# Optimization experiments

Measured on AMD Instinct MI355X. Metric: run time of the kernel, lower is better.

## Reference

```python
import jax, jax.numpy as jnp
import numpy as np
from jax import lax

STRIDES = (8, 16, 32)
NUM_CLASSES = 80
REG_MAX = 16
CONF_THR = 0.25
IOU_THR = 0.7
MAX_DET = 300
MAX_WH = 7680.0  # class-id offset for class-aware NMS


def setup_inputs() -> dict:
    key = jax.random.key(0)
    k1, k2, k3 = jax.random.split(key, 3)
    B = 32
    C = 4 * REG_MAX + NUM_CLASSES  # 144
    return {
        "p3": jax.random.normal(k1, (B, 80, 80, C), jnp.float32),
        "p4": jax.random.normal(k2, (B, 40, 40, C), jnp.float32),
        "p5": jax.random.normal(k3, (B, 20, 20, C), jnp.float32),
    }


def _make_anchors(shapes, strides):
    pts, strs = [], []
    for (h, w), s in zip(shapes, strides):
        sx = jnp.arange(w, dtype=jnp.float32) + 0.5
        sy = jnp.arange(h, dtype=jnp.float32) + 0.5
        gy, gx = jnp.meshgrid(sy, sx, indexing="ij")
        pts.append(jnp.stack([gx.ravel(), gy.ravel()], 0))  # (2, h*w)
        strs.append(jnp.full((h * w,), float(s), jnp.float32))
    return jnp.concatenate(pts, 1), jnp.concatenate(strs, 0)  # (2,A), (A,)


def _pairwise_iou(a, b):
    # a: (K,4) xyxy, b: (K,4) xyxy -> (K,K)
    lt = jnp.maximum(a[:, None, :2], b[None, :, :2])
    rb = jnp.minimum(a[:, None, 2:], b[None, :, 2:])
    wh = jnp.clip(rb - lt, 0.0)
    inter = wh[..., 0] * wh[..., 1]
    aa = (a[:, 2] - a[:, 0]) * (a[:, 3] - a[:, 1])
    ab = (b[:, 2] - b[:, 0]) * (b[:, 3] - b[:, 1])
    return inter / (aa[:, None] + ab[None, :] - inter + 1e-7)


def _nms_single(pred):
    # pred: (A, 4+nc) with boxes in xywh (center) format, scores sigmoid-activated
    xywh = pred[:, :4]
    scores = pred[:, 4:]
    best = jnp.max(scores, axis=-1)
    cls = jnp.argmax(scores, axis=-1)
    half = xywh[:, 2:] * 0.5
    boxes = jnp.concatenate([xywh[:, :2] - half, xywh[:, :2] + half], -1)  # xyxy
    score = jnp.where(best > CONF_THR, best, 0.0)
    top_s, idx = lax.top_k(score, MAX_DET)
    cbox = boxes[idx]                      # (K,4)
    ccls = cls[idx]                        # (K,)
    obox = cbox + ccls.astype(cbox.dtype)[:, None] * MAX_WH  # class-aware offset
    iou = _pairwise_iou(obox, obox)        # (K,K)
    k = jnp.arange(MAX_DET)

    def body(keep, i):
        suppressed = jnp.any(keep & (iou[i] > IOU_THR) & (k < i))
        ki = (top_s[i] > 0.0) & (~suppressed)
        return keep.at[i].set(ki), None

    keep, _ = lax.scan(body, jnp.zeros((MAX_DET,), bool), k)
    det = jnp.concatenate([cbox, top_s[:, None], ccls[:, None].astype(jnp.float32)], -1)
    return jnp.where(keep[:, None], det, 0.0)  # (K, 6): x1,y1,x2,y2,conf,cls


def _forward(p3, p4, p5):
    feats = [p3, p4, p5]
    shapes = [(f.shape[1], f.shape[2]) for f in feats]
    B = p3.shape[0]
    C = 4 * REG_MAX + NUM_CLASSES
    x = jnp.concatenate([f.reshape(B, -1, C) for f in feats], axis=1)  # (B, A, 144)
    box = x[:, :, : 4 * REG_MAX]   # (B, A, 64)
    cls = x[:, :, 4 * REG_MAX:]    # (B, A, 80)
    # DFL: split 64 channels into 4 sides x 16 bins, softmax over bins, expectation
    probs = jax.nn.softmax(box.reshape(B, -1, 4, REG_MAX), axis=-1)
    bins = jnp.arange(REG_MAX, dtype=jnp.float32)
    dist = jnp.einsum("bakr,r->bak", probs, bins)  # (B, A, 4) = l,t,r,b distances
    anchors, stride = _make_anchors(shapes, STRIDES)
    anc = anchors.T[None]  # (1, A, 2) anchor centers in grid units
    x1y1 = anc - dist[:, :, :2]
    x2y2 = anc + dist[:, :, 2:]
    dbox = jnp.concatenate([(x1y1 + x2y2) * 0.5, x2y2 - x1y1], -1) * stride[None, :, None]
    return jnp.concatenate([dbox, jax.nn.sigmoid(cls)], -1)  # (B, A, 84)


def reference(p3, p4, p5):
    pred = _forward(p3, p4, p5)
    return jax.vmap(_nms_single)(pred)  # (B, MAX_DET, 6)
```

## Files before the change

### kernel.cpp

```cpp
#include <hip/hip_runtime.h>
#include <math.h>

#define NUM_CLASSES 80
#define REG_MAX 16
#define NCH 144
#define A_TOT 8400
#define BATCH 32
#define MAX_DET 300
#define CONF_THR 0.25f
#define IOU_THR 0.7f
#define MAX_WH 7680.0f
#define CAP 1024
#define NBINS 1024
#define MASK_W 10
#define MROW 324

__global__ __launch_bounds__(256) void score_kernel(
    const float* __restrict__ p3, const float* __restrict__ p4,
    const float* __restrict__ p5,
    float* __restrict__ scores, int* __restrict__ clsArr)
{
    const int t = blockIdx.x * 256 + threadIdx.x;
    const int g = t >> 2;
    const int p = t & 3;
    const int b = g / A_TOT;
    const int a = g - b * A_TOT;

    const float* src;
    if (a < 6400)      src = p3 + ((size_t)b * 6400 + a) * NCH;
    else if (a < 8000) src = p4 + ((size_t)b * 1600 + (a - 6400)) * NCH;
    else               src = p5 + ((size_t)b * 400  + (a - 8000)) * NCH;

    const float4* s4 = (const float4*)src;
    float best = -INFINITY;
    int cbest = p * 4;
    #pragma unroll
    for (int q = 0; q < 5; ++q) {
        float4 c4 = s4[16 + q * 4 + p];
        int c = q * 16 + p * 4;
        if (c4.x > best) { best = c4.x; cbest = c + 0; }
        if (c4.y > best) { best = c4.y; cbest = c + 1; }
        if (c4.z > best) { best = c4.z; cbest = c + 2; }
        if (c4.w > best) { best = c4.w; cbest = c + 3; }
    }
    #pragma unroll
    for (int d = 1; d < 4; d <<= 1) {
        float ob = __shfl_xor(best, d, 64);
        int   oc = __shfl_xor(cbest, d, 64);
        if (ob > best || (ob == best && oc < cbest)) { best = ob; cbest = oc; }
    }

    if (p == 0) {
        float sig = 1.0f / (1.0f + expf(-best));
        scores[g] = (sig > CONF_THR) ? sig : 0.0f;
        clsArr[g] = cbest;
    }
}

__global__ __launch_bounds__(1024, 4) void nms_fused_kernel(
    const float* __restrict__ p3, const float* __restrict__ p4,
    const float* __restrict__ p5,
    const float* __restrict__ scores, const int* __restrict__ clsArr,
    float* __restrict__ out)
{
    __shared__ float sc_l[A_TOT];
    __shared__ unsigned hist[NBINS];
    __shared__ unsigned wtot[16];
    __shared__ unsigned woff[16];
    __shared__ unsigned long long cand[CAP];
    __shared__ unsigned long long sortedK[MAX_DET];
    __shared__ float4 cbox4[MAX_DET];
    __shared__ float4 obox4[MAX_DET];
    __shared__ float oarea[MAX_DET];
    __shared__ float tops[MAX_DET];
    __shared__ float tcls[MAX_DET];
    __shared__ unsigned mask[MASK_W][MROW];
    __shared__ unsigned aliveW[MASK_W];
    __shared__ unsigned keepW[MASK_W];
    __shared__ int bstar;
    __shared__ unsigned cnt;

    const int b = blockIdx.x;
    const int tid = threadIdx.x;
    const int lane = tid & 63;
    const int wv = tid >> 6;
    const float* sc = scores + (size_t)b * A_TOT;
    const int* cl = clsArr + (size_t)b * A_TOT;

    hist[tid] = 0;
    if (tid < MAX_DET) sortedK[tid] = 0ULL;
    if (tid == 0) { cnt = 0u; bstar = 0; }
    __syncthreads();

    #pragma unroll
    for (int k = 0; k < 9; ++k) {
        int i = tid + k * 1024;
        if (i < A_TOT) {
            float s = sc[i];
            sc_l[i] = s;
            if (s > 0.0f) {
                int bin = min((int)(s * (float)NBINS), NBINS - 1);
                atomicAdd(&hist[bin], 1u);
            }
        }
    }
    __syncthreads();

    unsigned v = hist[tid];
    #pragma unroll
    for (int d = 1; d < 64; d <<= 1) {
        unsigned o = __shfl_down(v, d, 64);
        if (lane + d < 64) v += o;
    }
    if (lane == 0) wtot[wv] = v;
    __syncthreads();
    if (tid < 16) {
        unsigned u = wtot[tid];
        unsigned t2 = u;
        #pragma unroll
        for (int d = 1; d < 16; d <<= 1) {
            unsigned o = __shfl_down(t2, d, 64);
            if (tid + d < 16) t2 += o;
        }
        woff[tid] = t2 - u;
    }
    __syncthreads();
    unsigned suff = v + woff[wv];
    hist[tid] = suff;
    __syncthreads();

    if (hist[tid] >= MAX_DET && (tid == NBINS - 1 || hist[tid + 1] < MAX_DET))
        bstar = tid;
    __syncthreads();
    const int bs = bstar;

    #pragma unroll
    for (int k = 0; k < 9; ++k) {
        int i = tid + k * 1024;
        float s = (i < A_TOT) ? sc_l[i] : 0.0f;
        bool pass = false;
        if (s > 0.0f) {
            int bin = min((int)(s * (float)NBINS), NBINS - 1);
            pass = (bin >= bs);
        }
        unsigned long long mb = __ballot(pass);
        unsigned nw = (unsigned)__popcll(mb);
        unsigned base = 0u;
        if (lane == 0) base = nw ? atomicAdd(&cnt, nw) : 0u;
        base = __shfl(base, 0, 64);
        if (pass) {
            unsigned off = (unsigned)__popcll(mb & ((1ULL << lane) - 1ULL));
            unsigned pos = base + off;
            if (pos < CAP) {
                unsigned sb = __float_as_uint(s);
                cand[pos] = ((unsigned long long)sb << 32) |
                            (unsigned long long)(0xFFFFFFFFu - (unsigned)i);
            }
        }
    }
    __syncthreads();

    const int n = min((int)cnt, CAP);
    if (tid < n) {
        unsigned long long mykey = cand[tid];
        int r = 0;
        #pragma unroll 8
        for (int j = 0; j < n; ++j) r += (cand[j] > mykey) ? 1 : 0;
        if (r < MAX_DET) sortedK[r] = mykey;
    }
    __syncthreads();

    const int gbase = lane & ~3;
    #pragma unroll
    for (int sweep = 0; sweep < 2; ++sweep) {
        int det = sweep * 256 + (tid >> 2);
        int p = tid & 3;
        unsigned long long key = (det < MAX_DET) ? sortedK[det] : 0ULL;
        float distp = 0.0f;
        unsigned i = 0xFFFFFFFFu - (unsigned)(key & 0xFFFFFFFFull);

        if (key != 0ULL) {
            const float* rowp;
            if (i < 6400)      rowp = p3 + ((size_t)b * 6400 + i) * NCH;
            else if (i < 8000) rowp = p4 + ((size_t)b * 1600 + (i - 6400)) * NCH;
            else               rowp = p5 + ((size_t)b * 400  + (i - 8000)) * NCH;
            const float4* s4 = (const float4*)rowp;
            float vv[16];
            float4 r0 = s4[p * 4 + 0];
            float4 r1 = s4[p * 4 + 1];
            float4 r2 = s4[p * 4 + 2];
            float4 r3 = s4[p * 4 + 3];
            vv[0]=r0.x; vv[1]=r0.y; vv[2]=r0.z; vv[3]=r0.w;
            vv[4]=r1.x; vv[5]=r1.y; vv[6]=r1.z; vv[7]=r1.w;
            vv[8]=r2.x; vv[9]=r2.y; vv[10]=r2.z; vv[11]=r2.w;
            vv[12]=r3.x; vv[13]=r3.y; vv[14]=r3.z; vv[15]=r3.w;
            float m = vv[0];
            #pragma unroll
            for (int k = 1; k < 16; ++k) m = fmaxf(m, vv[k]);
            float ssum = 0.0f, wsum = 0.0f;
            #pragma unroll
            for (int k = 0; k < 16; ++k) {
                float e = expf(vv[k] - m);
                ssum += e;
                wsum += e * (float)k;
            }
            distp = wsum / ssum;
        }
        float d0 = __shfl(distp, gbase + 0, 64);
        float d1 = __shfl(distp, gbase + 1, 64);
        float d2 = __shfl(distp, gbase + 2, 64);
        float d3 = __shfl(distp, gbase + 3, 64);

        if (det < MAX_DET && p == 0) {
            float s = __uint_as_float((unsigned)(key >> 32));
            tops[det] = s;
            float4 bb = make_float4(0.f, 0.f, 0.f, 0.f);
            float4 ob = bb;
            float cf = 0.0f;
            if (key != 0ULL) {
                int gyi, gxi; float strd;
                if (i < 6400)      { gyi = i / 80; gxi = i - gyi * 80; strd = 8.0f; }
                else if (i < 8000) { int li = i - 6400; gyi = li / 40; gxi = li - gyi * 40; strd = 16.0f; }
                else               { int li = i - 8000; gyi = li / 20; gxi = li - gyi * 20; strd = 32.0f; }
                float gx = (float)gxi + 0.5f;
                float gy = (float)gyi + 0.5f;
                float x1 = gx - d0, y1 = gy - d1;
                float x2 = gx + d2, y2 = gy + d3;
                float cx = ((x1 + x2) * 0.5f) * strd;
                float cy = ((y1 + y2) * 0.5f) * strd;
                float bw = (x2 - x1) * strd;
                float bh = (y2 - y1) * strd;
                float hx = bw * 0.5f, hy = bh * 0.5f;
                bb = make_float4(cx - hx, cy - hy, cx + hx, cy + hy);
                cf = (float)cl[i];
                float off = cf * MAX_WH;
                ob = make_float4(bb.x + off, bb.y + off, bb.z + off, bb.w + off);
            }
            cbox4[det] = bb;
            obox4[det] = ob;
            tcls[det] = cf;
            oarea[det] = (ob.z - ob.x) * (ob.w - ob.y);
        }
    }
    __syncthreads();

    for (int task = tid; task < MASK_W * MAX_DET; task += 1024) {
        int w = task / MAX_DET;
        int i = task - w * MAX_DET;
        float4 a = obox4[i];
        float aa = oarea[i];
        unsigned bits = 0;
        int j0 = w * 32;
        int jend = min(32, MAX_DET - j0);
        for (int jj = 0; jj < jend; ++jj) {
            int j = j0 + jj;
            float4 bo = obox4[j];
            float ab = oarea[j];
            float lx = fmaxf(a.x, bo.x), ly = fmaxf(a.y, bo.y);
            float rx = fminf(a.z, bo.z), ry = fminf(a.w, bo.w);
            float iw = fmaxf(rx - lx, 0.0f), ih = fmaxf(ry - ly, 0.0f);
            float inter = iw * ih;
            float iou = inter / (aa + ab - inter + 1e-7f);
            if (iou > IOU_THR) bits |= (1u << jj);
        }
        mask[w][i] = bits;
    }
    if (tid < MASK_W) {
        unsigned a = 0u;
        #pragma unroll
        for (int ii = 0; ii < 32; ++ii) {
            int i = tid * 32 + ii;
            if (i < MAX_DET && tops[i] > 0.0f) a |= (1u << ii);
        }
        aliveW[tid] = a;
    }
    __syncthreads();

    if (tid < 64) {
        unsigned supp = 0u;
        for (int w = 0; w < MASK_W; ++w) {
            unsigned suppcur = __shfl(supp, w, 64);
            unsigned aw = aliveW[w];
            unsigned m[32];
            #pragma unroll
            for (int q = 0; q < 8; ++q) {
                uint4 mq = *(const uint4*)&mask[w][w * 32 + q * 4];
                m[q*4+0] = mq.x; m[q*4+1] = mq.y;
                m[q*4+2] = mq.z; m[q*4+3] = mq.w;
            }
            unsigned kw = 0u;
            #pragma unroll
            for (int ii = 0; ii < 32; ++ii) {
                if (w * 32 + ii < MAX_DET) {
                    bool live = ((aw >> ii) & 1u) && !((suppcur >> ii) & 1u);
                    if (live) { suppcur |= m[ii]; kw |= (1u << ii); }
                }
            }
            if (tid == 0) keepW[w] = kw;
            if (tid < MASK_W) {
                unsigned acc = 0u;
                #pragma unroll
                for (int ii = 0; ii < 32; ++ii) {
                    if ((kw >> ii) & 1u) acc |= mask[tid][w * 32 + ii];
                }
                supp |= acc;
            }
        }
    }
    __syncthreads();

    float* ob = out + (size_t)b * MAX_DET * 6;
    for (int e = tid; e < MAX_DET * 6; e += 1024) {
        int i = e / 6, c = e - (e / 6) * 6;
        float val = 0.0f;
        if ((keepW[i >> 5] >> (i & 31)) & 1u) {
            if (c < 4)        val = (&cbox4[i].x)[c];
            else if (c == 4)  val = tops[i];
            else              val = tcls[i];
        }
        ob[e] = val;
    }
}

extern "C" void kernel_launch(void* const* d_in, const int* in_sizes, int n_in,
                              void* d_out, int out_size, void* d_ws, size_t ws_size,
                              hipStream_t stream) {
    const float* p3 = (const float*)d_in[0];
    const float* p4 = (const float*)d_in[1];
    const float* p5 = (const float*)d_in[2];
    float* out = (float*)d_out;

    char* base = (char*)d_ws;
    float* scores = (float*)base;
    int*   cls    = (int*)(base + 1075200);

    score_kernel<<<4200, 256, 0, stream>>>(p3, p4, p5, scores, cls);
    nms_fused_kernel<<<BATCH, 1024, 0, stream>>>(p3, p4, p5, scores, cls, out);
}
```

Measured before the change: 74.17 us.

## Split top-k selection into per-chunk local top-300 kernel plus merge-rank

Replaces the per-image histogram threshold and candidate rank sort inside the single NMS block with a new kernel. That kernel splits each image's 8400 scores into 8 chunks and computes a local top-300 per chunk by O(n^2) rank counting across 256 blocks. The NMS kernel then merges the 8 sorted lists by binary-search ranking. The aim is to spread top-k work across many more blocks than the 32 used before, at the cost of an extra kernel launch, a global round-trip of 8x300 keys per image, and quadratic comparisons per chunk.

Measured after the change: 122.3 us. +64.9%, slower.

```diff
diff --git a/kernel.cpp b/kernel.cpp
--- a/kernel.cpp
+++ b/kernel.cpp
@@ -10,10 +10,11 @@
 #define CONF_THR 0.25f
 #define IOU_THR 0.7f
 #define MAX_WH 7680.0f
-#define CAP 1024
-#define NBINS 1024
 #define MASK_W 10
 #define MROW 324
+#define CHUNK 1050
+#define NCHUNK 8
+#define KPAD 1536
 
 __global__ __launch_bounds__(256) void score_kernel(
     const float* __restrict__ p3, const float* __restrict__ p4,
@@ -57,17 +58,66 @@
     }
 }
 
-__global__ __launch_bounds__(1024, 4) void nms_fused_kernel(
+__global__ __launch_bounds__(512) void localtop_kernel(
+    const float* __restrict__ scores,
+    unsigned long long* __restrict__ gloc)
+{
+    __shared__ unsigned long long keys[KPAD];
+    __shared__ unsigned long long sortedLoc[MAX_DET];
+
+    const int bid = blockIdx.x;
+    const int b = bid >> 3;
+    const int c = bid & 7;
+    const int tid = threadIdx.x;
+    const int base = c * CHUNK;
+    const float* sc = scores + (size_t)b * A_TOT + base;
+
+    #pragma unroll
+    for (int q = 0; q < 3; ++q) {
+        int i = tid + q * 512;
+        unsigned long long k = 0ULL;
+        if (i < CHUNK) {
+            float s = sc[i];
+            if (s > 0.0f) {
+                unsigned sb = __float_as_uint(s);
+                unsigned gi = (unsigned)(base + i);
+                k = ((unsigned long long)sb << 32) |
+                    (unsigned long long)(0xFFFFFFFFu - gi);
+            }
+        }
+        keys[i] = k;
+    }
+    if (tid < MAX_DET) sortedLoc[tid] = 0ULL;
+    __syncthreads();
+
+    unsigned long long mk0 = keys[tid];
+    unsigned long long mk1 = keys[tid + 512];
+    unsigned long long mk2 = keys[tid + 1024];
+    int r0 = 0, r1 = 0, r2 = 0;
+    #pragma unroll 4
+    for (int j = 0; j < CHUNK; ++j) {
+        unsigned long long kj = keys[j];
+        r0 += (kj > mk0) ? 1 : 0;
+        r1 += (kj > mk1) ? 1 : 0;
+        r2 += (kj > mk2) ? 1 : 0;
+    }
+    if (mk0 != 0ULL && r0 < MAX_DET) sortedLoc[r0] = mk0;
+    if (mk1 != 0ULL && r1 < MAX_DET) sortedLoc[r1] = mk1;
+    if (mk2 != 0ULL && r2 < MAX_DET) sortedLoc[r2] = mk2;
+    __syncthreads();
+
+    unsigned long long* dst = gloc + ((size_t)b * NCHUNK + c) * MAX_DET;
+    if (tid < MAX_DET) dst[tid] = sortedLoc[tid];
+}
+
+__global__ __launch_bounds__(1024, 4) void nms_merge_kernel(
     const float* __restrict__ p3, const float* __restrict__ p4,
     const float* __restrict__ p5,
-    const float* __restrict__ scores, const int* __restrict__ clsArr,
+    const int* __restrict__ clsArr,
+    const unsigned long long* __restrict__ gloc,
     float* __restrict__ out)
 {
-    __shared__ float sc_l[A_TOT];
-    __shared__ unsigned hist[NBINS];
-    __shared__ unsigned wtot[16];
-    __shared__ unsigned woff[16];
-    __shared__ unsigned long long cand[CAP];
+    __shared__ unsigned long long lists[NCHUNK][MAX_DET];
     __shared__ unsigned long long sortedK[MAX_DET];
     __shared__ float4 cbox4[MAX_DET];
     __shared__ float4 obox4[MAX_DET];
@@ -77,96 +127,37 @@
     __shared__ unsigned mask[MASK_W][MROW];
     __shared__ unsigned aliveW[MASK_W];
     __shared__ unsigned keepW[MASK_W];
-    __shared__ int bstar;
-    __shared__ unsigned cnt;
 
     const int b = blockIdx.x;
     const int tid = threadIdx.x;
     const int lane = tid & 63;
-    const int wv = tid >> 6;
-    const float* sc = scores + (size_t)b * A_TOT;
     const int* cl = clsArr + (size_t)b * A_TOT;
-
-    hist[tid] = 0;
+    const unsigned long long* gl = gloc + (size_t)b * NCHUNK * MAX_DET;
+
+    for (int i = tid; i < NCHUNK * MAX_DET; i += 1024)
+        ((unsigned long long*)lists)[i] = gl[i];
     if (tid < MAX_DET) sortedK[tid] = 0ULL;
-    if (tid == 0) { cnt = 0u; bstar = 0; }
-    __syncthreads();
-
-    #pragma unroll
-    for (int k = 0; k < 9; ++k) {
-        int i = tid + k * 1024;
-        if (i < A_TOT) {
-            float s = sc[i];
-            sc_l[i] = s;
-            if (s > 0.0f) {
-                int bin = min((int)(s * (float)NBINS), NBINS - 1);
-                atomicAdd(&hist[bin], 1u);
-            }
-        }
-    }
-    __syncthreads();
-
-    unsigned v = hist[tid];
-    #pragma unroll
-    for (int d = 1; d < 64; d <<= 1) {
-        unsigned o = __shfl_down(v, d, 64);
-        if (lane + d < 64) v += o;
-    }
-    if (lane == 0) wtot[wv] = v;
-    __syncthreads();
-    if (tid < 16) {
-        unsigned u = wtot[tid];
-        unsigned t2 = u;
-        #pragma unroll
-        for (int d = 1; d < 16; d <<= 1) {
-            unsigned o = __shfl_down(t2, d, 64);
-            if (tid + d < 16) t2 += o;
-        }
-        woff[tid] = t2 - u;
-    }
-    __syncthreads();
-    unsigned suff = v + woff[wv];
-    hist[tid] = suff;
-    __syncthreads();
-
-    if (hist[tid] >= MAX_DET && (tid == NBINS - 1 || hist[tid + 1] < MAX_DET))
-        bstar = tid;
-    __syncthreads();
-    const int bs = bstar;
-
-    #pragma unroll
-    for (int k = 0; k < 9; ++k) {
-        int i = tid + k * 1024;
-        float s = (i < A_TOT) ? sc_l[i] : 0.0f;
-        bool pass = false;
-        if (s > 0.0f) {
-            int bin = min((int)(s * (float)NBINS), NBINS - 1);
-            pass = (bin >= bs);
-        }
-        unsigned long long mb = __ballot(pass);
-        unsigned nw = (unsigned)__popcll(mb);
-        unsigned base = 0u;
-        if (lane == 0) base = nw ? atomicAdd(&cnt, nw) : 0u;
-        base = __shfl(base, 0, 64);
-        if (pass) {
-            unsigned off = (unsigned)__popcll(mb & ((1ULL << lane) - 1ULL));
-            unsigned pos = base + off;
-            if (pos < CAP) {
-                unsigned sb = __float_as_uint(s);
-                cand[pos] = ((unsigned long long)sb << 32) |
-                            (unsigned long long)(0xFFFFFFFFu - (unsigned)i);
-            }
-        }
-    }
-    __syncthreads();
-
-    const int n = min((int)cnt, CAP);
-    if (tid < n) {
-        unsigned long long mykey = cand[tid];
-        int r = 0;
-        #pragma unroll 8
-        for (int j = 0; j < n; ++j) r += (cand[j] > mykey) ? 1 : 0;
-        if (r < MAX_DET) sortedK[r] = mykey;
+    __syncthreads();
+
+    for (int s = tid; s < NCHUNK * MAX_DET; s += 1024) {
+        int c = s / MAX_DET;
+        int r = s - c * MAX_DET;
+        unsigned long long k = lists[c][r];
+        if (k != 0ULL) {
+            int rank = r;
+            #pragma unroll
+            for (int c2 = 0; c2 < NCHUNK; ++c2) {
+                if (c2 != c) {
+                    int lo = 0, hi = MAX_DET;
+                    while (lo < hi) {
+                        int mid = (lo + hi) >> 1;
+                        if (lists[c2][mid] > k) lo = mid + 1; else hi = mid;
+                    }
+                    rank += lo;
+                }
+            }
+            if (rank < MAX_DET) sortedK[rank] = k;
+        }
     }
     __syncthreads();
 
@@ -196,13 +187,13 @@
             vv[12]=r3.x; vv[13]=r3.y; vv[14]=r3.z; vv[15]=r3.w;
             float m = vv[0];
             #pragma unroll
-            for (int k = 1; k < 16; ++k) m = fmaxf(m, vv[k]);
+            for (int k2 = 1; k2 < 16; ++k2) m = fmaxf(m, vv[k2]);
             float ssum = 0.0f, wsum = 0.0f;
             #pragma unroll
-            for (int k = 0; k < 16; ++k) {
-                float e = expf(vv[k] - m);
+            for (int k2 = 0; k2 < 16; ++k2) {
+                float e = expf(vv[k2] - m);
                 ssum += e;
-                wsum += e * (float)k;
+                wsum += e * (float)k2;
             }
             distp = wsum / ssum;
         }
@@ -331,9 +322,11 @@
     float* out = (float*)d_out;
 
     char* base = (char*)d_ws;
-    float* scores = (float*)base;
-    int*   cls    = (int*)(base + 1075200);
+    float*              scores = (float*)base;
+    int*                cls    = (int*)(base + 1075200);
+    unsigned long long* gloc   = (unsigned long long*)(base + 2150400);
 
     score_kernel<<<4200, 256, 0, stream>>>(p3, p4, p5, scores, cls);
-    nms_fused_kernel<<<BATCH, 1024, 0, stream>>>(p3, p4, p5, scores, cls, out);
+    localtop_kernel<<<BATCH * NCHUNK, 512, 0, stream>>>(scores, gloc);
+    nms_merge_kernel<<<BATCH, 1024, 0, stream>>>(p3, p4, p5, cls, gloc, out);
 }
```
